# Kernel tuning notes

Hardware: AMD Instinct MI355X
Metric: run time of the kernel (lower is better)

## Reference

```python
import jax, jax.numpy as jnp
import numpy as np

E, H, L, B = 2048, 32, 1024, 4
S = E // H  # 64
DM, DD = 32, 64


def _ln(x, w, b, eps=1e-5):
    m = x.mean(-1, keepdims=True)
    v = ((x - m) ** 2).mean(-1, keepdims=True)
    return (x - m) / jnp.sqrt(v + eps) * w + b


def setup_inputs() -> dict:
    key = jax.random.key(0)
    ks = jax.random.split(key, 24)
    sc = 0.02  # weight scale for stability
    d = {
        'x': jax.random.normal(ks[0], (B, L, E), jnp.float32),
        'state': jax.random.normal(ks[1], (B, 2 + S, E), jnp.float32) * 0.1,
        'ln1_w': jnp.ones((E,), jnp.float32), 'ln1_b': jnp.zeros((E,), jnp.float32),
        'ln2_w': jnp.ones((E,), jnp.float32), 'ln2_b': jnp.zeros((E,), jnp.float32),
        'maa_x': jax.random.normal(ks[2], (E,), jnp.float32) * 0.1,
        'maa_w1': jax.random.normal(ks[3], (E, 5 * DM), jnp.float32) * sc,
        'maa_w2': jax.random.normal(ks[4], (5, DM, E), jnp.float32) * sc,
        'maa_stack': jax.random.normal(ks[5], (1, 5, E), jnp.float32) * 0.1,
        'time_decay': jax.random.normal(ks[6], (E,), jnp.float32) * 0.5,
        'td_w1': jax.random.normal(ks[7], (E, DD), jnp.float32) * sc,
        'td_w2': jax.random.normal(ks[8], (DD, E), jnp.float32) * sc,
        'u': jax.random.normal(ks[9], (H, S, 1), jnp.float32) * 0.1,
        'Wr': jax.random.normal(ks[10], (E, E), jnp.float32) * sc,
        'Wk': jax.random.normal(ks[11], (E, E), jnp.float32) * sc,
        'Wv': jax.random.normal(ks[12], (E, E), jnp.float32) * sc,
        'Wg': jax.random.normal(ks[13], (E, E), jnp.float32) * sc,
        'Wo': jax.random.normal(ks[14], (E, E), jnp.float32) * sc,
        'gn_w': jnp.ones((E,), jnp.float32), 'gn_b': jnp.zeros((E,), jnp.float32),
        'ffn_maa_k': jax.random.normal(ks[15], (E,), jnp.float32) * 0.1,
        'ffn_maa_r': jax.random.normal(ks[16], (E,), jnp.float32) * 0.1,
        'Wfk': jax.random.normal(ks[17], (E, E), jnp.float32) * sc,
        'Wfr': jax.random.normal(ks[18], (E, E), jnp.float32) * sc,
        'Wfv': jax.random.normal(ks[19], (E, E), jnp.float32) * sc,
    }
    return d


def _block(x, state, ln1_w, ln1_b, ln2_w, ln2_b, maa_x, maa_w1, maa_w2, maa_stack,
           time_decay, td_w1, td_w2, u, Wr, Wk, Wv, Wg, Wo, gn_w, gn_b,
           ffn_maa_k, ffn_maa_r, Wfk, Wfr, Wfv):
    b, l, e = x.shape
    h = u.shape[0]
    s_ = e // h
    # ---- time mixing (parallel over L, sequential WKV scan) ----
    xa = _ln(x, ln1_w, ln1_b)
    # token shift: sx[t] = x[t-1] - x[t], seeded from state row 1
    sx = jnp.concatenate([state[:, 1:2] - xa[:, :1], xa[:, :-1] - xa[:, 1:]], axis=1)
    xxx = jnp.tanh((xa + sx * maa_x) @ maa_w1).reshape(b, l, 5, DM)
    xxx = jnp.einsum('blfd,fde->blfe', xxx, maa_w2)            # [B,L,5,E]
    xm = xa[:, :, None] + sx[:, :, None] * (maa_stack + xxx)   # [B,L,5,E]
    xk, xw, xv, xr, xg = (xm[:, :, j] for j in range(5))       # stack order: k,w,v,r,g
    w = jnp.exp(-jnp.exp(time_decay + jnp.tanh(xw @ td_w1) @ td_w2)).reshape(b, l, h, s_)
    r = (xr @ Wr.T).reshape(b, l, h, s_)
    k = (xk @ Wk.T).reshape(b, l, h, s_)
    v = (xv @ Wv.T).reshape(b, l, h, s_)
    g = jax.nn.silu(xg @ Wg.T)                                 # [B,L,E]
    s0 = state[:, 2:2 + s_].reshape(b, h, s_, s_)              # per-head WKV state

    def step(s, rkvw):
        r_t, k_t, v_t, w_t = rkvw                              # each [B,H,S]
        a = k_t[..., :, None] * v_t[..., None, :]              # outer product [B,H,S,S]
        out = jnp.einsum('bhi,bhij->bhj', r_t, u * a + s)      # [B,H,S]
        s = a + w_t[..., :, None] * s
        return s, out

    rkvw = tuple(jnp.moveaxis(t, 1, 0) for t in (r, k, v, w))  # [L,B,H,S]
    _, out = jax.lax.scan(step, s0, rkvw)
    out = jnp.moveaxis(out, 0, 1).reshape(b, l, e)             # [B,L,E]
    # group norm over heads (eps=1e-5)
    og = out.reshape(b, l, h, s_)
    m = og.mean(-1, keepdims=True)
    va = ((og - m) ** 2).mean(-1, keepdims=True)
    og = ((og - m) / jnp.sqrt(va + 1e-5)).reshape(b, l, e) * gn_w + gn_b
    x1 = x + (og * g) @ Wo.T
    # ---- channel mixing ----
    xc = _ln(x1, ln2_w, ln2_b)
    sx2 = jnp.concatenate([state[:, 0:1] - xc[:, :1], xc[:, :-1] - xc[:, 1:]], axis=1)
    xk2 = xc + sx2 * ffn_maa_k
    xr2 = xc + sx2 * ffn_maa_r
    rr = jax.nn.sigmoid(xr2 @ Wfr.T)
    kk = jnp.square(jax.nn.relu(xk2 @ Wfk.T))
    return x1 + rr * (kk @ Wfv.T)


def reference(x, state, ln1_w, ln1_b, ln2_w, ln2_b, maa_x, maa_w1, maa_w2, maa_stack,
              time_decay, td_w1, td_w2, u, Wr, Wk, Wv, Wg, Wo, gn_w, gn_b,
              ffn_maa_k, ffn_maa_r, Wfk, Wfr, Wfv):
    return _block(x, state, ln1_w, ln1_b, ln2_w, ln2_b, maa_x, maa_w1, maa_w2, maa_stack,
                  time_decay, td_w1, td_w2, u, Wr, Wk, Wv, Wg, Wo, gn_w, gn_b,
                  ffn_maa_k, ffn_maa_r, Wfk, Wfr, Wfv)
```

## Files before the change

### kernel.cpp

```cpp
#include <hip/hip_runtime.h>


#define E     2048
#define LL    1024
#define HHH   32
#define SSS   64
#define NBL   4096
#define NBLE  8388608

typedef short bf16x8 __attribute__((ext_vector_type(8)));
typedef float f32x4  __attribute__((ext_vector_type(4)));
using u16 = unsigned short;

__device__ __forceinline__ u16 f2b(float f) {
    union { float f; unsigned int u; } c; c.f = f;
    unsigned int u = c.u;
    unsigned int r = (u + 0x7fffu + ((u >> 16) & 1u)) >> 16;
    return (u16)r;
}
__device__ __forceinline__ float b2f(u16 b) {
    union { unsigned int u; float f; } c; c.u = ((unsigned int)b) << 16; return c.f;
}

__device__ __forceinline__ float wave_sum(float v) {
#pragma unroll
    for (int m = 32; m >= 1; m >>= 1) v += __shfl_xor(v, m, 64);
    return v;
}

__device__ __forceinline__ void gl_lds16(const void* g, void* l) {
    __builtin_amdgcn_global_load_lds((const __attribute__((address_space(1))) unsigned int*)g,
                                     (__attribute__((address_space(3))) unsigned int*)l, 16, 0, 0);
}


__global__ __launch_bounds__(256) void k_convert(const float* __restrict__ in,
                                                 u16* __restrict__ out, int n) {
    int i = (blockIdx.x * 256 + threadIdx.x) * 4;
    if (i >= n) return;
    float4 v = *reinterpret_cast<const float4*>(in + i);
    ushort4 o = make_ushort4(f2b(v.x), f2b(v.y), f2b(v.z), f2b(v.w));
    *reinterpret_cast<ushort4*>(out + i) = o;
}

__global__ __launch_bounds__(256) void k_transpose(const float* __restrict__ in,
                                                   u16* __restrict__ out, int R, int C) {
    int i = blockIdx.x * 256 + threadIdx.x;
    if (i >= R * C) return;
    int r = i / C, c = i - r * C;
    out[c * R + r] = f2b(in[i]);
}

__global__ __launch_bounds__(256) void k_ln(const float* __restrict__ x,
                                            const float* __restrict__ w,
                                            const float* __restrict__ b,
                                            float* __restrict__ out) {
    int row = blockIdx.x, tid = threadIdx.x;
    const float* xr = x + (size_t)row * E + tid * 8;
    float4 v0 = *reinterpret_cast<const float4*>(xr);
    float4 v1 = *reinterpret_cast<const float4*>(xr + 4);
    float s = v0.x + v0.y + v0.z + v0.w + v1.x + v1.y + v1.z + v1.w;
    __shared__ float red[4];
    s = wave_sum(s);
    int wid = tid >> 6, lane = tid & 63;
    if (lane == 0) red[wid] = s;
    __syncthreads();
    float mean = (red[0] + red[1] + red[2] + red[3]) * (1.0f / E);
    __syncthreads();
    float q = 0.f;
    q += (v0.x - mean) * (v0.x - mean); q += (v0.y - mean) * (v0.y - mean);
    q += (v0.z - mean) * (v0.z - mean); q += (v0.w - mean) * (v0.w - mean);
    q += (v1.x - mean) * (v1.x - mean); q += (v1.y - mean) * (v1.y - mean);
    q += (v1.z - mean) * (v1.z - mean); q += (v1.w - mean) * (v1.w - mean);
    q = wave_sum(q);
    if (lane == 0) red[wid] = q;
    __syncthreads();
    float inv = rsqrtf((red[0] + red[1] + red[2] + red[3]) * (1.0f / E) + 1e-5f);
    int e = tid * 8;
    float4 w0 = *reinterpret_cast<const float4*>(w + e);
    float4 w1 = *reinterpret_cast<const float4*>(w + e + 4);
    float4 b0 = *reinterpret_cast<const float4*>(b + e);
    float4 b1 = *reinterpret_cast<const float4*>(b + e + 4);
    float4 o0, o1;
    o0.x = (v0.x - mean) * inv * w0.x + b0.x; o0.y = (v0.y - mean) * inv * w0.y + b0.y;
    o0.z = (v0.z - mean) * inv * w0.z + b0.z; o0.w = (v0.w - mean) * inv * w0.w + b0.w;
    o1.x = (v1.x - mean) * inv * w1.x + b1.x; o1.y = (v1.y - mean) * inv * w1.y + b1.y;
    o1.z = (v1.z - mean) * inv * w1.z + b1.z; o1.w = (v1.w - mean) * inv * w1.w + b1.w;
    float* op = out + (size_t)row * E + e;
    *reinterpret_cast<float4*>(op) = o0;
    *reinterpret_cast<float4*>(op + 4) = o1;
}

__global__ __launch_bounds__(256) void k_mk(const float* __restrict__ xa,
                                            const float* __restrict__ state,
                                            const float* __restrict__ maa_x,
                                            u16* __restrict__ out) {
    int i = (blockIdx.x * 256 + threadIdx.x) * 4;
    if (i >= NBLE) return;
    int n = i >> 11, e = i & (E - 1);
    int l = n & (LL - 1), b = n >> 10;
    float4 cur = *reinterpret_cast<const float4*>(xa + i);
    float4 prev;
    if (l > 0) prev = *reinterpret_cast<const float4*>(xa + i - E);
    else       prev = *reinterpret_cast<const float4*>(state + (size_t)b * 66 * E + E + e);
    float4 m = *reinterpret_cast<const float4*>(maa_x + e);
    ushort4 o = make_ushort4(f2b(cur.x + (prev.x - cur.x) * m.x),
                             f2b(cur.y + (prev.y - cur.y) * m.y),
                             f2b(cur.z + (prev.z - cur.z) * m.z),
                             f2b(cur.w + (prev.w - cur.w) * m.w));
    *reinterpret_cast<ushort4*>(out + i) = o;
}

__global__ __launch_bounds__(256) void k_mix2(const float* __restrict__ xc,
                                              const float* __restrict__ state,
                                              const float* __restrict__ mk,
                                              const float* __restrict__ mr,
                                              u16* __restrict__ xk2,
                                              u16* __restrict__ xr2) {
    int i = (blockIdx.x * 256 + threadIdx.x) * 4;
    if (i >= NBLE) return;
    int n = i >> 11, e = i & (E - 1);
    int l = n & (LL - 1), b = n >> 10;
    float4 cur = *reinterpret_cast<const float4*>(xc + i);
    float4 prev;
    if (l > 0) prev = *reinterpret_cast<const float4*>(xc + i - E);
    else       prev = *reinterpret_cast<const float4*>(state + (size_t)b * 66 * E + e);
    float4 sx = make_float4(prev.x - cur.x, prev.y - cur.y, prev.z - cur.z, prev.w - cur.w);
    float4 k4 = *reinterpret_cast<const float4*>(mk + e);
    float4 r4 = *reinterpret_cast<const float4*>(mr + e);
    ushort4 ok = make_ushort4(f2b(cur.x + sx.x * k4.x), f2b(cur.y + sx.y * k4.y),
                              f2b(cur.z + sx.z * k4.z), f2b(cur.w + sx.w * k4.w));
    ushort4 orr = make_ushort4(f2b(cur.x + sx.x * r4.x), f2b(cur.y + sx.y * r4.y),
                               f2b(cur.z + sx.z * r4.z), f2b(cur.w + sx.w * r4.w));
    *reinterpret_cast<ushort4*>(xk2 + i) = ok;
    *reinterpret_cast<ushort4*>(xr2 + i) = orr;
}

__global__ __launch_bounds__(256) void k_gnorm(const float* __restrict__ wkv,
                                               const u16* __restrict__ g,
                                               const float* __restrict__ gw,
                                               const float* __restrict__ gb,
                                               u16* __restrict__ ogg) {
    int gidx = blockIdx.x * 4 + (threadIdx.x >> 6);
    int lane = threadIdx.x & 63;
    int n = gidx >> 5, h = gidx & 31;
    size_t base = (size_t)n * E + h * SSS;
    float v = wkv[base + lane];
    float mean = wave_sum(v) * (1.0f / SSS);
    float d = v - mean;
    float var = wave_sum(d * d) * (1.0f / SSS);
    float norm = d * rsqrtf(var + 1e-5f);
    int e = h * SSS + lane;
    float res = norm * gw[e] + gb[e];
    float gv = b2f(g[base + lane]);
    ogg[base + lane] = f2b(res * gv);
}

#define CT 16

__global__ __launch_bounds__(256) void k_scan(const u16* __restrict__ Rb,
                                              const u16* __restrict__ Kb,
                                              const u16* __restrict__ Vb,
                                              const float* __restrict__ W,
                                              const float* __restrict__ state,
                                              const float* __restrict__ u,
                                              float* __restrict__ out) {
    __shared__ u16   ldsR[2][CT * 64];
    __shared__ u16   ldsK[2][CT * 64];
    __shared__ float ldsW[2][CT * 64];
    __shared__ u16   ldsV[2][CT * 16];
    const int blk = blockIdx.x;
    const int bh = blk & 127;
    const int jq = blk >> 7;
    const int b = bh >> 5, h = bh & 31;
    const int tid = threadIdx.x;
    const int wvid = tid >> 6;
    const int lane = tid & 63;
    const int ig = lane >> 2;
    const int jl = lane & 3;
    const int jv = wvid * 4 + jl;
    const int j  = jq * 16 + jv;
    const int i0 = ig * 4;
    float s[4], uu[4];
    const float* s0 = state + (size_t)b * 66 * E + 2 * E + h * (SSS * SSS);
#pragma unroll
    for (int ii = 0; ii < 4; ii++) {
        s[ii] = s0[(i0 + ii) * SSS + j];
        uu[ii] = u[h * SSS + i0 + ii];
    }
    const size_t off0 = (size_t)b * LL * E + h * SSS;

    auto stage = [&](int c, int bufsel) {
        size_t base = off0 + (size_t)c * CT * E;
        if (wvid == 0) {
            const u16* g0 = Rb + base + (size_t)(lane >> 3) * E + ((lane & 7) << 3);
            gl_lds16(g0,         &ldsR[bufsel][lane * 8]);
            gl_lds16(g0 + 8 * E, &ldsR[bufsel][512 + lane * 8]);
            if (lane < 32) {
                const u16* gv = Vb + base + (size_t)(lane >> 1) * E + jq * 16 + ((lane & 1) << 3);
                gl_lds16(gv, &ldsV[bufsel][lane * 8]);
            }
        } else if (wvid == 1) {
            const u16* g0 = Kb + base + (size_t)(lane >> 3) * E + ((lane & 7) << 3);
            gl_lds16(g0,         &ldsK[bufsel][lane * 8]);
            gl_lds16(g0 + 8 * E, &ldsK[bufsel][512 + lane * 8]);
        } else if (wvid == 2) {
            const float* g0 = W + base + (size_t)(lane >> 4) * E + ((lane & 15) << 2);
            gl_lds16(g0,         &ldsW[bufsel][lane * 4]);
            gl_lds16(g0 + 4 * E, &ldsW[bufsel][256 + lane * 4]);
        } else {
            const float* g0 = W + base + (size_t)(8 + (lane >> 4)) * E + ((lane & 15) << 2);
            gl_lds16(g0,         &ldsW[bufsel][512 + lane * 4]);
            gl_lds16(g0 + 4 * E, &ldsW[bufsel][768 + lane * 4]);
        }
    };

    stage(0, 0);
    __syncthreads();
    int cur = 0;
    for (int c = 0; c < LL / CT; c++) {
        if (c + 1 < LL / CT) stage(c + 1, cur ^ 1);
        float accs[CT];
#pragma unroll
        for (int tt = 0; tt < CT; tt++) {
            ushort4 rv = *reinterpret_cast<const ushort4*>(&ldsR[cur][tt * 64 + i0]);
            ushort4 kv = *reinterpret_cast<const ushort4*>(&ldsK[cur][tt * 64 + i0]);
            float4  wv = *reinterpret_cast<const float4*>(&ldsW[cur][tt * 64 + i0]);
            float vj = b2f(ldsV[cur][tt * 16 + jv]);
            float acc = 0.f, a;
            a = b2f(kv.x) * vj; acc += b2f(rv.x) * fmaf(uu[0], a, s[0]); s[0] = fmaf(wv.x, s[0], a);
            a = b2f(kv.y) * vj; acc += b2f(rv.y) * fmaf(uu[1], a, s[1]); s[1] = fmaf(wv.y, s[1], a);
            a = b2f(kv.z) * vj; acc += b2f(rv.z) * fmaf(uu[2], a, s[2]); s[2] = fmaf(wv.z, s[2], a);
            a = b2f(kv.w) * vj; acc += b2f(rv.w) * fmaf(uu[3], a, s[3]); s[3] = fmaf(wv.w, s[3], a);
            accs[tt] = acc;
        }
#pragma unroll
        for (int tt = 0; tt < CT; tt++) accs[tt] += __shfl_xor(accs[tt], 4, 64);
#pragma unroll
        for (int tt = 0; tt < CT; tt++) accs[tt] += __shfl_xor(accs[tt], 8, 64);
#pragma unroll
        for (int tt = 0; tt < CT; tt++) accs[tt] += __shfl_xor(accs[tt], 16, 64);
#pragma unroll
        for (int tt = 0; tt < CT; tt++) accs[tt] += __shfl_xor(accs[tt], 32, 64);
        if (ig == 0) {
            size_t offt = off0 + (size_t)c * CT * E + j;
#pragma unroll
            for (int tt = 0; tt < CT; tt++) out[offt + (size_t)tt * E] = accs[tt];
        }
        __syncthreads();
        cur ^= 1;
    }
}

template <int EP>
__global__ __launch_bounds__(512, 2) void k_gemm256(const u16* __restrict__ A,
                                                    const u16* __restrict__ Bw,
                                                    void* __restrict__ C,
                                                    const float* __restrict__ emat1,
                                                    const float* __restrict__ emat2) {
    __shared__ u16 As[3][256 * 64];
    __shared__ u16 Bs[3][128 * 64];
    const int tid = threadIdx.x;
    const int bid = blockIdx.x;
    const int sw = (bid & 7) * 32 + (bid >> 3);
    const int m0 = (sw >> 4) << 8;
    const int n0 = (sw & 15) << 7;
    const int srow = tid >> 3;
    const int schunk = (tid & 7) ^ (srow & 7);
    const u16* gA = A + (size_t)(m0 + srow) * E + schunk * 8;
    const u16* gB = Bw + (size_t)(n0 + srow) * E + schunk * 8;

    const int wv = tid >> 6, lane = tid & 63;
    const int wm = wv >> 1, wn = wv & 1;
    const int lr = lane & 15, lq = lane >> 4;
    const int c0 = ((lq ^ (lr & 7)) << 3);
    const int c1 = (((4 + lq) ^ (lr & 7)) << 3);
    const int arow = wm * 64 + lr;
    const int brow = wn * 64 + lr;

    f32x4 acc[4][4];
#pragma unroll
    for (int mt = 0; mt < 4; mt++)
#pragma unroll
        for (int nt = 0; nt < 4; nt++) acc[mt][nt] = {0.f, 0.f, 0.f, 0.f};

    const int NT = E / 64;

    auto stage_full = [&](int kt, int buf) {
        const u16* a = gA + kt * 64;
        const u16* b = gB + kt * 64;
        u16* la = &As[buf][0] + tid * 8;
        u16* lb = &Bs[buf][0] + tid * 8;
        gl_lds16(a,                   la);
        gl_lds16(a + (size_t)64  * E, la + 64 * 64);
        gl_lds16(a + (size_t)128 * E, la + 128 * 64);
        gl_lds16(a + (size_t)192 * E, la + 192 * 64);
        gl_lds16(b,                   lb);
        gl_lds16(b + (size_t)64  * E, lb + 64 * 64);
    };

    stage_full(0, 0);
    stage_full(1, 1);
    asm volatile("s_waitcnt vmcnt(6)" ::: "memory");
    __builtin_amdgcn_s_barrier();

    for (int kt = 0; kt < NT; kt++) {
        const int rb = kt % 3;
        const int sb = (kt + 2) % 3;
        const bool st = (kt + 2) < NT;
        const u16* as = &As[rb][0];
        const u16* bs = &Bs[rb][0];
        const u16* ga = gA + (kt + 2) * 64;
        const u16* gb = gB + (kt + 2) * 64;
        u16* la = &As[sb][0] + tid * 8;
        u16* lb = &Bs[sb][0] + tid * 8;
        bf16x8 a0, a1, b0[4], b1[4];

        a0 = *reinterpret_cast<const bf16x8*>(as + (arow +  0) * 64 + c0);
        a1 = *reinterpret_cast<const bf16x8*>(as + (arow + 16) * 64 + c0);
#pragma unroll
        for (int nt = 0; nt < 4; nt++)
            b0[nt] = *reinterpret_cast<const bf16x8*>(bs + (brow + nt * 16) * 64 + c0);
        if (st) { gl_lds16(ga, la); gl_lds16(ga + (size_t)64 * E, la + 64 * 64); }
        __builtin_amdgcn_s_barrier();
        asm volatile("s_waitcnt lgkmcnt(0)" ::: "memory");
        __builtin_amdgcn_s_setprio(1);
#pragma unroll
        for (int nt = 0; nt < 4; nt++) {
            acc[0][nt] = __builtin_amdgcn_mfma_f32_16x16x32_bf16(a0, b0[nt], acc[0][nt], 0, 0, 0);
            acc[1][nt] = __builtin_amdgcn_mfma_f32_16x16x32_bf16(a1, b0[nt], acc[1][nt], 0, 0, 0);
        }
        __builtin_amdgcn_s_setprio(0);
        __builtin_amdgcn_s_barrier();

        a0 = *reinterpret_cast<const bf16x8*>(as + (arow +  0) * 64 + c1);
        a1 = *reinterpret_cast<const bf16x8*>(as + (arow + 16) * 64 + c1);
#pragma unroll
        for (int nt = 0; nt < 4; nt++)
            b1[nt] = *reinterpret_cast<const bf16x8*>(bs + (brow + nt * 16) * 64 + c1);
        if (st) { gl_lds16(ga + (size_t)128 * E, la + 128 * 64); gl_lds16(ga + (size_t)192 * E, la + 192 * 64); }
        __builtin_amdgcn_s_barrier();
        asm volatile("s_waitcnt lgkmcnt(0)" ::: "memory");
        __builtin_amdgcn_s_setprio(1);
#pragma unroll
        for (int nt = 0; nt < 4; nt++) {
            acc[0][nt] = __builtin_amdgcn_mfma_f32_16x16x32_bf16(a0, b1[nt], acc[0][nt], 0, 0, 0);
            acc[1][nt] = __builtin_amdgcn_mfma_f32_16x16x32_bf16(a1, b1[nt], acc[1][nt], 0, 0, 0);
        }
        __builtin_amdgcn_s_setprio(0);
        __builtin_amdgcn_s_barrier();

        a0 = *reinterpret_cast<const bf16x8*>(as + (arow + 32) * 64 + c0);
        a1 = *reinterpret_cast<const bf16x8*>(as + (arow + 48) * 64 + c0);
        if (st) { gl_lds16(gb, lb); gl_lds16(gb + (size_t)64 * E, lb + 64 * 64); }
        __builtin_amdgcn_s_barrier();
        asm volatile("s_waitcnt lgkmcnt(0)" ::: "memory");
        __builtin_amdgcn_s_setprio(1);
#pragma unroll
        for (int nt = 0; nt < 4; nt++) {
            acc[2][nt] = __builtin_amdgcn_mfma_f32_16x16x32_bf16(a0, b0[nt], acc[2][nt], 0, 0, 0);
            acc[3][nt] = __builtin_amdgcn_mfma_f32_16x16x32_bf16(a1, b0[nt], acc[3][nt], 0, 0, 0);
        }
        __builtin_amdgcn_s_setprio(0);
        __builtin_amdgcn_s_barrier();

        a0 = *reinterpret_cast<const bf16x8*>(as + (arow + 32) * 64 + c1);
        a1 = *reinterpret_cast<const bf16x8*>(as + (arow + 48) * 64 + c1);
        if (st) asm volatile("s_waitcnt vmcnt(6)" ::: "memory");
        else    asm volatile("s_waitcnt vmcnt(0)" ::: "memory");
        __builtin_amdgcn_s_barrier();
        asm volatile("s_waitcnt lgkmcnt(0)" ::: "memory");
        __builtin_amdgcn_s_setprio(1);
#pragma unroll
        for (int nt = 0; nt < 4; nt++) {
            acc[2][nt] = __builtin_amdgcn_mfma_f32_16x16x32_bf16(a0, b1[nt], acc[2][nt], 0, 0, 0);
            acc[3][nt] = __builtin_amdgcn_mfma_f32_16x16x32_bf16(a1, b1[nt], acc[3][nt], 0, 0, 0);
        }
        __builtin_amdgcn_s_setprio(0);
        __builtin_amdgcn_s_barrier();
    }

    const int gmb = m0 + wm * 64 + (lq << 2);
    const int gnb = n0 + wn * 64 + lr;
#pragma unroll
    for (int mt = 0; mt < 4; mt++) {
#pragma unroll
        for (int nt = 0; nt < 4; nt++) {
            int gn = gnb + nt * 16;
#pragma unroll
            for (int i = 0; i < 4; i++) {
                int gm = gmb + mt * 16 + i;
                size_t idx = (size_t)gm * E + gn;
                float v = acc[mt][nt][i];
                if constexpr (EP == 5) ((float*)C)[idx] = emat1[idx] + v;
                else if constexpr (EP == 6) ((float*)C)[idx] = 1.f / (1.f + expf(-v));
                else if constexpr (EP == 7) { float t = fmaxf(v, 0.f); ((u16*)C)[idx] = f2b(t * t); }
                else if constexpr (EP == 8) ((float*)C)[idx] = emat1[idx] + emat2[idx] * v;
                else if constexpr (EP == 9) ((u16*)C)[idx] = f2b(v);
                else if constexpr (EP == 10) { float sg = 1.f / (1.f + expf(-v)); ((u16*)C)[idx] = f2b(v * sg); }
            }
        }
    }
}

template <int EP>
__global__ __launch_bounds__(256) void k_gemm128(const u16* __restrict__ A, int lda,
                                                 const u16* __restrict__ Bw,
                                                 void* __restrict__ C, int K,
                                                 const float* __restrict__ evec,
                                                 const float* __restrict__ emat1,
                                                 const float* __restrict__ emat2) {
    __shared__ u16 As[128 * 32];
    __shared__ u16 Bs[128 * 32];
    const int tid = threadIdx.x;
    const int m0 = blockIdx.y << 7, n0 = blockIdx.x << 7;
    const int srow = tid >> 2;
    const int scol = (((tid & 3) ^ ((srow >> 1) & 3)) << 3);
    const int wv = tid >> 6, lane = tid & 63;
    const int wy = (wv >> 1) << 6, wx = (wv & 1) << 6;
    const int lr = lane & 15, lq = lane >> 4;
    const int cofs = ((lq ^ ((lr >> 1) & 3)) << 3);
    f32x4 acc[4][4];
#pragma unroll
    for (int a = 0; a < 4; a++)
#pragma unroll
        for (int bq = 0; bq < 4; bq++) acc[a][bq] = {0.f, 0.f, 0.f, 0.f};
    const u16* gA = A + (size_t)(m0 + srow) * lda + scol;
    const u16* gB = Bw + (size_t)(n0 + srow) * K + scol;
    u16* lA = As + srow * 32 + ((tid & 3) << 3);
    u16* lB = Bs + srow * 32 + ((tid & 3) << 3);
    for (int k0 = 0; k0 < K; k0 += 32) {
        gl_lds16(gA + k0, lA);
        gl_lds16(gA + (size_t)64 * lda + k0, lA + 64 * 32);
        gl_lds16(gB + k0, lB);
        gl_lds16(gB + (size_t)64 * K + k0, lB + 64 * 32);
        __syncthreads();
        bf16x8 af[4], bfr[4];
#pragma unroll
        for (int mt = 0; mt < 4; mt++)
            af[mt] = *reinterpret_cast<const bf16x8*>(As + (wy + mt * 16 + lr) * 32 + cofs);
#pragma unroll
        for (int nt = 0; nt < 4; nt++)
            bfr[nt] = *reinterpret_cast<const bf16x8*>(Bs + (wx + nt * 16 + lr) * 32 + cofs);
#pragma unroll
        for (int mt = 0; mt < 4; mt++)
#pragma unroll
            for (int nt = 0; nt < 4; nt++)
                acc[mt][nt] = __builtin_amdgcn_mfma_f32_16x16x32_bf16(af[mt], bfr[nt], acc[mt][nt], 0, 0, 0);
        __syncthreads();
    }
    const int gmb = m0 + wy + (lq << 2);
    const int gnb = n0 + wx + lr;
#pragma unroll
    for (int mt = 0; mt < 4; mt++) {
#pragma unroll
        for (int nt = 0; nt < 4; nt++) {
            int gn = gnb + nt * 16;
#pragma unroll
            for (int i = 0; i < 4; i++) {
                int gm = gmb + mt * 16 + i;
                size_t idx = (size_t)gm * E + gn;
                float v = acc[mt][nt][i];
                if constexpr (EP == 2) {
                    int l = gm & (LL - 1), bb = gm >> 10;
                    float cur = emat1[idx];
                    float prev = (l > 0) ? emat1[idx - E]
                                         : emat2[(size_t)bb * 66 * E + E + gn];
                    ((u16*)C)[idx] = f2b(cur + (prev - cur) * (evec[gn] + v));
                }
                else if constexpr (EP == 3) ((float*)C)[idx] = expf(-expf(evec[gn] + v));
            }
        }
    }
}

#define BK  32
#define LDP 40

template <int EP>
__global__ __launch_bounds__(256) void k_gemm(const u16* __restrict__ A, int lda,
                                              const u16* __restrict__ Bw,
                                              void* __restrict__ C,
                                              int M, int N, int K) {
    __shared__ u16 As[64 * LDP];
    __shared__ u16 Bs[64 * LDP];
    const int tid = threadIdx.x;
    const int m0 = blockIdx.y << 6, n0 = blockIdx.x << 6;
    const int srow = tid >> 2, skc = (tid & 3) << 3;
    const int lane = tid & 63, wv = tid >> 6;
    const int wr = (wv >> 1) << 5, wc = (wv & 1) << 5;
    const int lr = lane & 15, lq = lane >> 4;
    f32x4 acc[2][2];
#pragma unroll
    for (int a = 0; a < 2; a++)
#pragma unroll
        for (int bq = 0; bq < 2; bq++) acc[a][bq] = {0.f, 0.f, 0.f, 0.f};
    const u16* aptr = A + (size_t)(m0 + srow) * lda + skc;
    const u16* bptr = Bw + (size_t)(n0 + srow) * K + skc;
    const bool bvalid = (n0 + srow) < N;
    for (int k0 = 0; k0 < K; k0 += BK) {
        float4 av = *reinterpret_cast<const float4*>(aptr + k0);
        float4 bv = bvalid ? *reinterpret_cast<const float4*>(bptr + k0)
                           : make_float4(0.f, 0.f, 0.f, 0.f);
        __syncthreads();
        *reinterpret_cast<float4*>(As + srow * LDP + skc) = av;
        *reinterpret_cast<float4*>(Bs + srow * LDP + skc) = bv;
        __syncthreads();
        bf16x8 a0 = *reinterpret_cast<const bf16x8*>(As + (wr + lr) * LDP + lq * 8);
        bf16x8 a1 = *reinterpret_cast<const bf16x8*>(As + (wr + 16 + lr) * LDP + lq * 8);
        bf16x8 b0 = *reinterpret_cast<const bf16x8*>(Bs + (wc + lr) * LDP + lq * 8);
        bf16x8 b1 = *reinterpret_cast<const bf16x8*>(Bs + (wc + 16 + lr) * LDP + lq * 8);
        acc[0][0] = __builtin_amdgcn_mfma_f32_16x16x32_bf16(a0, b0, acc[0][0], 0, 0, 0);
        acc[0][1] = __builtin_amdgcn_mfma_f32_16x16x32_bf16(a0, b1, acc[0][1], 0, 0, 0);
        acc[1][0] = __builtin_amdgcn_mfma_f32_16x16x32_bf16(a1, b0, acc[1][0], 0, 0, 0);
        acc[1][1] = __builtin_amdgcn_mfma_f32_16x16x32_bf16(a1, b1, acc[1][1], 0, 0, 0);
    }
    const int gmb = m0 + wr + lq * 4;
    const int gnb = n0 + wc + lr;
#pragma unroll
    for (int mi = 0; mi < 2; mi++) {
#pragma unroll
        for (int ni = 0; ni < 2; ni++) {
            int gn = gnb + ni * 16;
            if (gn >= N) continue;
#pragma unroll
            for (int i = 0; i < 4; i++) {
                int gm = gmb + mi * 16 + i;
                size_t idx = (size_t)gm * N + gn;
                float v = acc[mi][ni][i];
                if constexpr (EP == 1) ((u16*)C)[idx] = f2b(tanhf(v));
            }
        }
    }
}


extern "C" void kernel_launch(void* const* d_in, const int* in_sizes, int n_in,
                              void* d_out, int out_size, void* d_ws, size_t ws_size,
                              hipStream_t stream) {
    const float* x          = (const float*)d_in[0];
    const float* state      = (const float*)d_in[1];
    const float* ln1_w      = (const float*)d_in[2];
    const float* ln1_b      = (const float*)d_in[3];
    const float* ln2_w      = (const float*)d_in[4];
    const float* ln2_b      = (const float*)d_in[5];
    const float* maa_x      = (const float*)d_in[6];
    const float* maa_w1     = (const float*)d_in[7];
    const float* maa_w2     = (const float*)d_in[8];
    const float* maa_stack  = (const float*)d_in[9];
    const float* time_decay = (const float*)d_in[10];
    const float* td_w1      = (const float*)d_in[11];
    const float* td_w2      = (const float*)d_in[12];
    const float* u          = (const float*)d_in[13];
    const float* Wr         = (const float*)d_in[14];
    const float* Wk         = (const float*)d_in[15];
    const float* Wv         = (const float*)d_in[16];
    const float* Wg         = (const float*)d_in[17];
    const float* Wo         = (const float*)d_in[18];
    const float* gn_w       = (const float*)d_in[19];
    const float* gn_b       = (const float*)d_in[20];
    const float* ffn_k      = (const float*)d_in[21];
    const float* ffn_r      = (const float*)d_in[22];
    const float* Wfk        = (const float*)d_in[23];
    const float* Wfr        = (const float*)d_in[24];
    const float* Wfv        = (const float*)d_in[25];

    char* ws = (char*)d_ws;
    float* R0 = (float*)(ws);
    float* R1 = (float*)(ws + 33554432);
    u16*   R2 = (u16*)(ws + 67108864);
    u16*   R3 = (u16*)(ws + 83886080);
    u16*   R4 = (u16*)(ws + 100663296);
    u16*   R5 = (u16*)(ws + 117440512);
    u16*   R6 = (u16*)(ws + 134217728);
    u16*   WB = (u16*)(ws + 150994944);
    u16*   Hx = (u16*)(ws + 159383552);
    u16*   Ht = (u16*)(ws + 160694272);
    u16*  WT1 = (u16*)(ws + 161218560);
    u16*  WT2 = (u16*)(ws + 161873920);
    u16*  WT3 = (u16*)(ws + 162529280);
    u16*  WT4 = (u16*)(ws + 162791424);

    dim3 blk(256);
    dim3 blk512(512);
    dim3 g256(256);
    dim3 g128(16, 32);
    dim3 g160(3, 64), g64(1, 64);
    const int ncv = (E * E / 4) / 256;
    const int nel = NBLE / 1024;

    k_transpose<<<(E * 160 + 255) / 256, blk, 0, stream>>>(maa_w1, WT1, E, 160);
    for (int f = 0; f < 5; f++)
        k_transpose<<<(32 * E + 255) / 256, blk, 0, stream>>>(maa_w2 + f * 32 * E, WT2 + f * E * 32, 32, E);
    k_transpose<<<(E * 64 + 255) / 256, blk, 0, stream>>>(td_w1, WT3, E, 64);
    k_transpose<<<(64 * E + 255) / 256, blk, 0, stream>>>(td_w2, WT4, 64, E);

    k_ln<<<NBL, blk, 0, stream>>>(x, ln1_w, ln1_b, R0);
    k_mk<<<nel, blk, 0, stream>>>(R0, state, maa_x, R2);
    k_gemm<1><<<g160, blk, 0, stream>>>(R2, E, WT1, Hx, NBL, 160, E);

    k_gemm128<2><<<g128, blk, 0, stream>>>(Hx + 1 * 32, 160, WT2 + 1 * E * 32, R2, 32,
                                           maa_stack + 1 * E, R0, state);
    k_gemm<1><<<g64, blk, 0, stream>>>(R2, E, WT3, Ht, NBL, 64, E);
    k_gemm128<3><<<g128, blk, 0, stream>>>(Ht, 64, WT4, R1, 64, time_decay, nullptr, nullptr);

    k_gemm128<2><<<g128, blk, 0, stream>>>(Hx + 0 * 32, 160, WT2 + 0 * E * 32, R2, 32,
                                           maa_stack + 0 * E, R0, state);
    k_convert<<<ncv, blk, 0, stream>>>(Wk, WB, E * E);
    k_gemm256<9><<<g256, blk512, 0, stream>>>(R2, WB, R4, nullptr, nullptr);

    k_gemm128<2><<<g128, blk, 0, stream>>>(Hx + 2 * 32, 160, WT2 + 2 * E * 32, R2, 32,
                                           maa_stack + 2 * E, R0, state);
    k_convert<<<ncv, blk, 0, stream>>>(Wv, WB, E * E);
    k_gemm256<9><<<g256, blk512, 0, stream>>>(R2, WB, R5, nullptr, nullptr);

    k_gemm128<2><<<g128, blk, 0, stream>>>(Hx + 4 * 32, 160, WT2 + 4 * E * 32, R2, 32,
                                           maa_stack + 4 * E, R0, state);
    k_convert<<<ncv, blk, 0, stream>>>(Wg, WB, E * E);
    k_gemm256<10><<<g256, blk512, 0, stream>>>(R2, WB, R6, nullptr, nullptr);

    k_gemm128<2><<<g128, blk, 0, stream>>>(Hx + 3 * 32, 160, WT2 + 3 * E * 32, R2, 32,
                                           maa_stack + 3 * E, R0, state);
    k_convert<<<ncv, blk, 0, stream>>>(Wr, WB, E * E);
    k_gemm256<9><<<g256, blk512, 0, stream>>>(R2, WB, R3, nullptr, nullptr);

    k_scan<<<512, blk, 0, stream>>>(R3, R4, R5, R1, state, u, R0);
    k_gnorm<<<NBL * HHH / 4, blk, 0, stream>>>(R0, R6, gn_w, gn_b, R6);

    k_convert<<<ncv, blk, 0, stream>>>(Wo, WB, E * E);
    k_gemm256<5><<<g256, blk512, 0, stream>>>(R6, WB, R0, x, nullptr);

    k_ln<<<NBL, blk, 0, stream>>>(R0, ln2_w, ln2_b, R1);
    k_mix2<<<nel, blk, 0, stream>>>(R1, state, ffn_k, ffn_r, R2, R3);
    k_convert<<<ncv, blk, 0, stream>>>(Wfk, WB, E * E);
    k_gemm256<7><<<g256, blk512, 0, stream>>>(R2, WB, R4, nullptr, nullptr);
    k_convert<<<ncv, blk, 0, stream>>>(Wfr, WB, E * E);
    k_gemm256<6><<<g256, blk512, 0, stream>>>(R3, WB, R1, nullptr, nullptr);
    k_convert<<<ncv, blk, 0, stream>>>(Wfv, WB, E * E);
    k_gemm256<8><<<g256, blk512, 0, stream>>>(R4, WB, (float*)d_out, R0, R1);
}
```

Measured before the change: 1.035 ms.

## Halve scan block size, give each lane 8 state rows, reduce with DPP

The WKV scan kernel now runs 128 threads per block, and each lane holds 8 state rows instead of 4. That halves the cross-lane reduction to 8 lanes, done with DPP quad permutes and a ds_swizzle instead of four shfl_xor stages. Staging loads are spread evenly across all threads rather than split by wavefront role. Each step does more serial work per lane and fewer waves run per block, trading latency hiding for cheaper reductions and less lane redundancy.

```diff
diff --git a/kernel.cpp b/kernel.cpp
--- a/kernel.cpp
+++ b/kernel.cpp
@@ -31,6 +31,17 @@
 __device__ __forceinline__ void gl_lds16(const void* g, void* l) {
     __builtin_amdgcn_global_load_lds((const __attribute__((address_space(1))) unsigned int*)g,
                                      (__attribute__((address_space(3))) unsigned int*)l, 16, 0, 0);
+}
+
+template <int CTRL>
+__device__ __forceinline__ float dpp_mov(float v) {
+    int s = __builtin_bit_cast(int, v);
+    int r = __builtin_amdgcn_update_dpp(s, s, CTRL, 0xF, 0xF, false);
+    return __builtin_bit_cast(float, r);
+}
+__device__ __forceinline__ float swz_xor4(float v) {
+    int r = __builtin_amdgcn_ds_swizzle(__builtin_bit_cast(int, v), 0x101F);
+    return __builtin_bit_cast(float, r);
 }
 
 
@@ -158,7 +169,7 @@
 
 #define CT 16
 
-__global__ __launch_bounds__(256) void k_scan(const u16* __restrict__ Rb,
+__global__ __launch_bounds__(128) void k_scan(const u16* __restrict__ Rb,
                                               const u16* __restrict__ Kb,
                                               const u16* __restrict__ Vb,
                                               const float* __restrict__ W,
@@ -176,42 +187,32 @@
     const int tid = threadIdx.x;
     const int wvid = tid >> 6;
     const int lane = tid & 63;
-    const int ig = lane >> 2;
-    const int jl = lane & 3;
-    const int jv = wvid * 4 + jl;
+    const int ig = lane & 7;
+    const int jl = lane >> 3;
+    const int jv = wvid * 8 + jl;
     const int j  = jq * 16 + jv;
-    const int i0 = ig * 4;
-    float s[4], uu[4];
+    const int i0 = ig * 8;
+    float s[8], uu[8];
     const float* s0 = state + (size_t)b * 66 * E + 2 * E + h * (SSS * SSS);
 #pragma unroll
-    for (int ii = 0; ii < 4; ii++) {
-        s[ii] = s0[(i0 + ii) * SSS + j];
-        uu[ii] = u[h * SSS + i0 + ii];
+    for (int r = 0; r < 8; r++) {
+        s[r] = s0[(i0 + r) * SSS + j];
+        uu[r] = u[h * SSS + i0 + r];
     }
     const size_t off0 = (size_t)b * LL * E + h * SSS;
 
     auto stage = [&](int c, int bufsel) {
         size_t base = off0 + (size_t)c * CT * E;
-        if (wvid == 0) {
-            const u16* g0 = Rb + base + (size_t)(lane >> 3) * E + ((lane & 7) << 3);
-            gl_lds16(g0,         &ldsR[bufsel][lane * 8]);
-            gl_lds16(g0 + 8 * E, &ldsR[bufsel][512 + lane * 8]);
-            if (lane < 32) {
-                const u16* gv = Vb + base + (size_t)(lane >> 1) * E + jq * 16 + ((lane & 1) << 3);
-                gl_lds16(gv, &ldsV[bufsel][lane * 8]);
-            }
-        } else if (wvid == 1) {
-            const u16* g0 = Kb + base + (size_t)(lane >> 3) * E + ((lane & 7) << 3);
-            gl_lds16(g0,         &ldsK[bufsel][lane * 8]);
-            gl_lds16(g0 + 8 * E, &ldsK[bufsel][512 + lane * 8]);
-        } else if (wvid == 2) {
-            const float* g0 = W + base + (size_t)(lane >> 4) * E + ((lane & 15) << 2);
-            gl_lds16(g0,         &ldsW[bufsel][lane * 4]);
-            gl_lds16(g0 + 4 * E, &ldsW[bufsel][256 + lane * 4]);
-        } else {
-            const float* g0 = W + base + (size_t)(8 + (lane >> 4)) * E + ((lane & 15) << 2);
-            gl_lds16(g0,         &ldsW[bufsel][512 + lane * 4]);
-            gl_lds16(g0 + 4 * E, &ldsW[bufsel][768 + lane * 4]);
+        const u16* gR = Rb + base + (size_t)(tid >> 3) * E + ((tid & 7) << 3);
+        gl_lds16(gR, &ldsR[bufsel][tid * 8]);
+        const u16* gK = Kb + base + (size_t)(tid >> 3) * E + ((tid & 7) << 3);
+        gl_lds16(gK, &ldsK[bufsel][tid * 8]);
+        const float* gW = W + base + (size_t)(tid >> 4) * E + ((tid & 15) << 2);
+        gl_lds16(gW,         &ldsW[bufsel][tid * 4]);
+        gl_lds16(gW + 8 * E, &ldsW[bufsel][512 + tid * 4]);
+        if (tid < 32) {
+            const u16* gV = Vb + base + (size_t)(tid >> 1) * E + jq * 16 + ((tid & 1) << 3);
+            gl_lds16(gV, &ldsV[bufsel][tid * 8]);
         }
     };
 
@@ -223,25 +224,28 @@
         float accs[CT];
 #pragma unroll
         for (int tt = 0; tt < CT; tt++) {
-            ushort4 rv = *reinterpret_cast<const ushort4*>(&ldsR[cur][tt * 64 + i0]);
-            ushort4 kv = *reinterpret_cast<const ushort4*>(&ldsK[cur][tt * 64 + i0]);
-            float4  wv = *reinterpret_cast<const float4*>(&ldsW[cur][tt * 64 + i0]);
+            bf16x8 rv = *reinterpret_cast<const bf16x8*>(&ldsR[cur][tt * 64 + i0]);
+            bf16x8 kv = *reinterpret_cast<const bf16x8*>(&ldsK[cur][tt * 64 + i0]);
+            float4  w0 = *reinterpret_cast<const float4*>(&ldsW[cur][tt * 64 + i0]);
+            float4  w1 = *reinterpret_cast<const float4*>(&ldsW[cur][tt * 64 + i0 + 4]);
             float vj = b2f(ldsV[cur][tt * 16 + jv]);
             float acc = 0.f, a;
-            a = b2f(kv.x) * vj; acc += b2f(rv.x) * fmaf(uu[0], a, s[0]); s[0] = fmaf(wv.x, s[0], a);
-            a = b2f(kv.y) * vj; acc += b2f(rv.y) * fmaf(uu[1], a, s[1]); s[1] = fmaf(wv.y, s[1], a);
-            a = b2f(kv.z) * vj; acc += b2f(rv.z) * fmaf(uu[2], a, s[2]); s[2] = fmaf(wv.z, s[2], a);
-            a = b2f(kv.w) * vj; acc += b2f(rv.w) * fmaf(uu[3], a, s[3]); s[3] = fmaf(wv.w, s[3], a);
+            a = b2f((u16)kv[0]) * vj; acc += b2f((u16)rv[0]) * fmaf(uu[0], a, s[0]); s[0] = fmaf(w0.x, s[0], a);
+            a = b2f((u16)kv[1]) * vj; acc += b2f((u16)rv[1]) * fmaf(uu[1], a, s[1]); s[1] = fmaf(w0.y, s[1], a);
+            a = b2f((u16)kv[2]) * vj; acc += b2f((u16)rv[2]) * fmaf(uu[2], a, s[2]); s[2] = fmaf(w0.z, s[2], a);
+            a = b2f((u16)kv[3]) * vj; acc += b2f((u16)rv[3]) * fmaf(uu[3], a, s[3]); s[3] = fmaf(w0.w, s[3], a);
+            a = b2f((u16)kv[4]) * vj; acc += b2f((u16)rv[4]) * fmaf(uu[4], a, s[4]); s[4] = fmaf(w1.x, s[4], a);
+            a = b2f((u16)kv[5]) * vj; acc += b2f((u16)rv[5]) * fmaf(uu[5], a, s[5]); s[5] = fmaf(w1.y, s[5], a);
+            a = b2f((u16)kv[6]) * vj; acc += b2f((u16)rv[6]) * fmaf(uu[6], a, s[6]); s[6] = fmaf(w1.z, s[6], a);
+            a = b2f((u16)kv[7]) * vj; acc += b2f((u16)rv[7]) * fmaf(uu[7], a, s[7]); s[7] = fmaf(w1.w, s[7], a);
             accs[tt] = acc;
         }
 #pragma unroll
-        for (int tt = 0; tt < CT; tt++) accs[tt] += __shfl_xor(accs[tt], 4, 64);
-#pragma unroll
-        for (int tt = 0; tt < CT; tt++) accs[tt] += __shfl_xor(accs[tt], 8, 64);
-#pragma unroll
-        for (int tt = 0; tt < CT; tt++) accs[tt] += __shfl_xor(accs[tt], 16, 64);
-#pragma unroll
-        for (int tt = 0; tt < CT; tt++) accs[tt] += __shfl_xor(accs[tt], 32, 64);
+        for (int tt = 0; tt < CT; tt++) accs[tt] += dpp_mov<0xB1>(accs[tt]);
+#pragma unroll
+        for (int tt = 0; tt < CT; tt++) accs[tt] += dpp_mov<0x4E>(accs[tt]);
+#pragma unroll
+        for (int tt = 0; tt < CT; tt++) accs[tt] = accs[tt] + swz_xor4(accs[tt]);
         if (ig == 0) {
             size_t offt = off0 + (size_t)c * CT * E + j;
 #pragma unroll
@@ -624,7 +628,7 @@
     k_convert<<<ncv, blk, 0, stream>>>(Wr, WB, E * E);
     k_gemm256<9><<<g256, blk512, 0, stream>>>(R2, WB, R3, nullptr, nullptr);
 
-    k_scan<<<512, blk, 0, stream>>>(R3, R4, R5, R1, state, u, R0);
+    k_scan<<<512, dim3(128), 0, stream>>>(R3, R4, R5, R1, state, u, R0);
     k_gnorm<<<NBL * HHH / 4, blk, 0, stream>>>(R0, R6, gn_w, gn_b, R6);
 
     k_convert<<<ncv, blk, 0, stream>>>(Wo, WB, E * E);
```

Result: slower. 1.166 ms (+12.6%).
